# Performance work log

Hardware: AMD Instinct MI355X
Metric: run time of the kernel (lower is better)

## Reference

```python
import jax, jax.numpy as jnp
import numpy as np

PS = 8          # patch size
D_STATE = 16
D_CONV = 4
DT_RANK = 6     # ceil(96/16)
N_HEADS = 2
NEG = jnp.float32(-1e30)
_DIRS = np.array([[-1, 0], [1, 0], [0, -1], [0, 1]], np.int32)


def _ln(x, w, b, eps=1e-5):
    mu = x.mean(-1, keepdims=True)
    var = ((x - mu) ** 2).mean(-1, keepdims=True)
    return (x - mu) * jax.lax.rsqrt(var + eps) * w + b


def _vit_score_map(x, pos_embed, proj_w, proj_b, in_w, in_b, out_w, out_b,
                   ln1_w, ln1_b, ff1_w, ff1_b, ff2_w, ff2_b, ln2_w, ln2_b,
                   score_w, score_b):
    B, C, H, W = x.shape
    Hp, Wp = H // PS, W // PS
    N = Hp * Wp
    E = proj_w.shape[0]
    # F.unfold ordering: per patch the vector is (C, kr, kc) flattened
    patches = x.reshape(B, C, Hp, PS, Wp, PS).transpose(0, 2, 4, 1, 3, 5).reshape(B, N, C * PS * PS)
    patches = patches @ proj_w.T + proj_b
    if pos_embed.shape[1] != N:
        o = int(pos_embed.shape[1] ** 0.5)
        pe = jax.image.resize(pos_embed.reshape(1, o, o, E), (1, Hp, Wp, E), 'bilinear').reshape(1, N, E)
    else:
        pe = pos_embed
    patches = patches + 0.1 * pe
    # nn.TransformerEncoderLayer defaults: post-norm, ReLU, eval (no dropout)
    qkv = patches @ in_w.T + in_b
    q, k, v = jnp.split(qkv, 3, axis=-1)
    dh = E // N_HEADS
    def heads(t):
        return t.reshape(B, N, N_HEADS, dh).transpose(0, 2, 1, 3)
    q, k, v = heads(q), heads(k), heads(v)
    attn = jax.nn.softmax(jnp.einsum('bhqd,bhkd->bhqk', q, k) / np.float32(np.sqrt(dh)), axis=-1)
    ctx = jnp.einsum('bhqk,bhkd->bhqd', attn, v).transpose(0, 2, 1, 3).reshape(B, N, E)
    src = _ln(patches + (ctx @ out_w.T + out_b), ln1_w, ln1_b)
    ff = jax.nn.relu(src @ ff1_w.T + ff1_b) @ ff2_w.T + ff2_b
    src = _ln(src + ff, ln2_w, ln2_b)
    scores = jax.nn.sigmoid((src @ score_w.T + score_b)[..., 0])
    pvar = patches.var(axis=-1, ddof=1)          # torch.var is unbiased
    final = 0.7 * scores + 0.3 * jax.nn.sigmoid(pvar * 10.0)
    return final.reshape(B, Hp, Wp)


def _traversal(score):
    """Greedy adaptive patch traversal: start at global argmax, walk to the best
    unvisited 4-neighbor; on dead-end jump to the global argmax over unvisited."""
    Hp, Wp = score.shape
    n = Hp * Wp
    s = score.reshape(-1)
    dirs = jnp.asarray(_DIRS)
    start = jnp.argmax(s).astype(jnp.int32)
    visited0 = jnp.zeros((n,), bool).at[start].set(True)

    def step(carry, _):
        visited, cur = carry
        ci, cj = cur // Wp, cur % Wp
        ni, nj = ci + dirs[:, 0], cj + dirs[:, 1]
        valid = (ni >= 0) & (ni < Hp) & (nj >= 0) & (nj < Wp)
        nidx = (jnp.clip(ni, 0, Hp - 1) * Wp + jnp.clip(nj, 0, Wp - 1)).astype(jnp.int32)
        nsc = jnp.where(valid & ~visited[nidx], s[nidx], NEG)
        b = jnp.argmax(nsc)                       # first-max tie-break == '>' loop order
        jump = jnp.argmax(jnp.where(visited, NEG, s)).astype(jnp.int32)
        nxt = jnp.where(nsc[b] > NEG * 0.5, nidx[b], jump).astype(jnp.int32)
        return (visited.at[nxt].set(True), nxt), nxt

    _, rest = jax.lax.scan(step, (visited0, start), None, length=n - 1)
    return jnp.concatenate([start[None], rest])


def _mamba(u, in_w, conv_w, conv_b, xproj_w, dt_w, dt_b, A_log, D_skip, out_w):
    B, L, _ = u.shape
    d_in = conv_w.shape[0]
    xz = u @ in_w.T                               # (B,L,2*d_in)
    xx, z = jnp.split(xz, 2, axis=-1)
    # causal depthwise conv over sequence
    xc = jnp.pad(xx.transpose(0, 2, 1), ((0, 0), (0, 0), (D_CONV - 1, 0)))
    xc = jax.lax.conv_general_dilated(xc, conv_w, (1,), 'VALID',
                                      feature_group_count=d_in,
                                      dimension_numbers=('NCH', 'OIH', 'NCH'))
    xx = jax.nn.silu((xc + conv_b[None, :, None]).transpose(0, 2, 1))   # (B,L,d_in)
    dbl = xx @ xproj_w.T
    dt, Bm, Cm = jnp.split(dbl, [DT_RANK, DT_RANK + D_STATE], axis=-1)
    dt = jax.nn.softplus(dt @ dt_w.T + dt_b)      # (B,L,d_in)
    A = -jnp.exp(A_log)                           # (d_in, d_state)

    def step(h, inp):
        dt_t, B_t, C_t, x_t = inp                 # (B,d_in),(B,ds),(B,ds),(B,d_in)
        h = jnp.exp(dt_t[..., None] * A) * h + (dt_t * x_t)[..., None] * B_t[:, None, :]
        return h, jnp.einsum('bds,bs->bd', h, C_t)

    h0 = jnp.zeros((B, d_in, D_STATE), u.dtype)
    xs = (dt.transpose(1, 0, 2), Bm.transpose(1, 0, 2), Cm.transpose(1, 0, 2), xx.transpose(1, 0, 2))
    _, ys = jax.lax.scan(step, h0, xs)
    y = ys.transpose(1, 0, 2) + xx * D_skip
    return (y * jax.nn.silu(z)) @ out_w.T


def setup_inputs() -> dict:
    key = jax.random.key(0)
    ks = jax.random.split(key, 20)
    B, C, H, W = 2, 96, 128, 128
    E, FF = 96, 2048
    d_in, dr, ds, dc = 192, 6, 16, 4
    f32 = jnp.float32
    def w(k, shape, s=0.02):
        return jax.random.normal(k, shape, f32) * s
    return dict(
        x=jax.random.normal(ks[0], (B, C, H, W), f32),
        pe=w(ks[1], (B, H * W, C), 0.02),
        pos_embed=w(ks[2], (1, 784, E)),
        vit_proj_w=w(ks[3], (E, C * PS * PS)),
        vit_proj_b=jnp.zeros((E,), f32),
        attn_in_w=w(ks[4], (3 * E, E)),
        attn_in_b=jnp.zeros((3 * E,), f32),
        attn_out_w=w(ks[5], (E, E)),
        attn_out_b=jnp.zeros((E,), f32),
        ln1_w=jnp.ones((E,), f32), ln1_b=jnp.zeros((E,), f32),
        ff1_w=w(ks[6], (FF, E)), ff1_b=jnp.zeros((FF,), f32),
        ff2_w=w(ks[7], (E, FF)), ff2_b=jnp.zeros((E,), f32),
        ln2_w=jnp.ones((E,), f32), ln2_b=jnp.zeros((E,), f32),
        score_w=w(ks[8], (1, E)), score_b=jnp.zeros((1,), f32),
        norm_w=jnp.ones((C,), f32), norm_b=jnp.zeros((C,), f32),
        in_proj_w=w(ks[9], (2 * d_in, C)),
        conv_w=w(ks[10], (d_in, 1, dc), 0.1),
        conv_b=jnp.zeros((d_in,), f32),
        x_proj_w=w(ks[11], (dr + 2 * ds, d_in)),
        dt_w=w(ks[12], (d_in, dr)),
        dt_b=jnp.full((d_in,), -4.6, f32),        # softplus(dt_b) ~ 0.01 (mamba dt init)
        A_log=jnp.log(jnp.tile(jnp.arange(1, ds + 1, dtype=f32), (d_in, 1))),
        D_skip=jnp.ones((d_in,), f32),
        out_proj_w=w(ks[13], (C, d_in)),
    )


def reference(x, pe, pos_embed, vit_proj_w, vit_proj_b, attn_in_w, attn_in_b,
              attn_out_w, attn_out_b, ln1_w, ln1_b, ff1_w, ff1_b, ff2_w, ff2_b,
              ln2_w, ln2_b, score_w, score_b, norm_w, norm_b, in_proj_w,
              conv_w, conv_b, x_proj_w, dt_w, dt_b, A_log, D_skip, out_proj_w):
    B, C, H, W = x.shape
    n = H * W
    # Dynamic_Adaptive_Scan with the code's DCNv3Function-is-None fallback:
    # x = input_last, permuted back to channels-first => identity on x.
    x_adapted = x
    score_map = _vit_score_map(x_adapted, pos_embed, vit_proj_w, vit_proj_b,
                               attn_in_w, attn_in_b, attn_out_w, attn_out_b,
                               ln1_w, ln1_b, ff1_w, ff1_b, ff2_w, ff2_b,
                               ln2_w, ln2_b, score_w, score_b)
    order = jax.vmap(_traversal)(jax.lax.stop_gradient(score_map))    # (B, Hp*Wp)
    Hp, Wp = score_map.shape[1], score_map.shape[2]
    pi, pj = order // Wp, order % Wp
    # expand each patch into its PSxPS pixels in raster order
    offs = (jnp.arange(PS, dtype=jnp.int32)[:, None] * W + jnp.arange(PS, dtype=jnp.int32)[None, :]).reshape(-1)
    idx = ((pi * PS * W + pj * PS)[..., None] + offs).reshape(B, n)    # (B, n)
    x_tok = jnp.take_along_axis(x_adapted.reshape(B, C, n), idx[:, None, :], axis=2).transpose(0, 2, 1)
    pe_r = jnp.take_along_axis(pe, idx[..., None], axis=1)
    tokens = _ln(x_tok + pe_r, norm_w, norm_b)
    y = _mamba(tokens, in_proj_w, conv_w, conv_b, x_proj_w, dt_w, dt_b, A_log, D_skip, out_proj_w)
    # scatter back to spatial raster order
    out = jax.vmap(lambda yb, ib: jnp.zeros_like(yb).at[ib].set(yb))(y, idx)
    return out.transpose(0, 2, 1).reshape(B, C, H, W)
```

## Files before the change

### kernel.cpp

```cpp
#include <hip/hip_runtime.h>
#include <math.h>

#define BB 2
#define CC 96
#define HH 128
#define WW 128
#define PS 8
#define HP 16
#define WP 16
#define NPATCH 256
#define EE 96
#define FF 2048
#define DH 48
#define DIN 192
#define DR 6
#define DS 16
#define LL 16384
#define NCHUNK 512
#define CLEN 32
#define NSEG 16
#define SEGC 32
#define KTOT 6144
#define KSPLIT 32
#define KSL 192

__device__ __forceinline__ float sigmoid_acc(float x){ return 1.f/(1.f+expf(-x)); }
__device__ __forceinline__ float sigmoid_fast(float x){ return 1.f/(1.f+__expf(-x)); }

__global__ void k_resize_pe(const float* __restrict__ pos, float* __restrict__ pe16){
  int n = blockIdx.x;
  int oi = n / WP, oj = n % WP;
  int e = threadIdx.x;
  const float inv = 1.75f;
  float sfi = (oi + 0.5f)*inv - 0.5f;
  float sfj = (oj + 0.5f)*inv - 0.5f;
  int i0 = max(0, (int)ceilf(sfi - inv)), i1 = min(27, (int)floorf(sfi + inv));
  int j0 = max(0, (int)ceilf(sfj - inv)), j1 = min(27, (int)floorf(sfj + inv));
  float si = 0.f, sj = 0.f;
  for(int j=i0;j<=i1;j++) si += fmaxf(0.f, 1.f - fabsf(sfi - (float)j)/inv);
  for(int j=j0;j<=j1;j++) sj += fmaxf(0.f, 1.f - fabsf(sfj - (float)j)/inv);
  float acc = 0.f;
  for(int ji=i0;ji<=i1;ji++){
    float wv = fmaxf(0.f, 1.f - fabsf(sfi - (float)ji)/inv) / si;
    for(int jj=j0;jj<=j1;jj++){
      float wu = fmaxf(0.f, 1.f - fabsf(sfj - (float)jj)/inv);
      acc += wv * (wu/sj) * pos[(ji*28+jj)*EE + e];
    }
  }
  pe16[n*EE + e] = acc;
}

__global__ void k_wtr(const float* __restrict__ vw, float* __restrict__ Wt){
  __shared__ float t[64*97];
  int k0 = blockIdx.x*64;
  int tid = threadIdx.x;
  for(int i=tid;i<64*EE;i+=256){
    int e = i>>6, kk = i&63;
    t[kk*97 + e] = vw[(size_t)e*KTOT + k0 + kk];
  }
  __syncthreads();
  for(int i=tid;i<64*EE;i+=256){
    int kk = i/EE, e = i%EE;
    Wt[(size_t)(k0+kk)*EE + e] = t[kk*97 + e];
  }
}

__global__ __launch_bounds__(384) void k_pproj(const float* __restrict__ x,
    const float* __restrict__ Wt, float* __restrict__ part){
  __shared__ float As[16*196];
  int bidx = blockIdx.x;
  int ks = bidx & (KSPLIT-1);
  int pb = bidx >> 5;
  int b = pb >> 4, pi = pb & 15;
  int c0 = ks*3;
  int tid = threadIdx.x;
  for(int i=tid;i<24*128;i+=384){
    int row = i>>7;
    int col = i&127;
    int cl = row>>3, dr = row&7;
    float v = x[(((size_t)(b*CC + c0+cl))<<14) + (size_t)((pi*PS+dr)<<7) + col];
    As[(col>>3)*196 + cl*64 + dr*8 + (col&7)] = v;
  }
  __syncthreads();
  int e = tid % EE;
  int pq = tid / EE;
  const float* wp = Wt + (size_t)(ks*KSL)*EE + e;
  float acc0=0.f, acc1=0.f, acc2=0.f, acc3=0.f;
  const float4* A0 = (const float4*)(As + (pq*4+0)*196);
  const float4* A1 = (const float4*)(As + (pq*4+1)*196);
  const float4* A2 = (const float4*)(As + (pq*4+2)*196);
  const float4* A3 = (const float4*)(As + (pq*4+3)*196);
  #pragma unroll 4
  for(int k4=0;k4<48;k4++){
    float w0 = wp[(k4*4+0)*EE];
    float w1 = wp[(k4*4+1)*EE];
    float w2 = wp[(k4*4+2)*EE];
    float w3 = wp[(k4*4+3)*EE];
    float4 a;
    a = A0[k4]; acc0 += a.x*w0 + a.y*w1 + a.z*w2 + a.w*w3;
    a = A1[k4]; acc1 += a.x*w0 + a.y*w1 + a.z*w2 + a.w*w3;
    a = A2[k4]; acc2 += a.x*w0 + a.y*w1 + a.z*w2 + a.w*w3;
    a = A3[k4]; acc3 += a.x*w0 + a.y*w1 + a.z*w2 + a.w*w3;
  }
  size_t gp0 = (size_t)b*NPATCH + pi*WP + pq*4;
  part[((size_t)ks*512 + gp0+0)*EE + e] = acc0;
  part[((size_t)ks*512 + gp0+1)*EE + e] = acc1;
  part[((size_t)ks*512 + gp0+2)*EE + e] = acc2;
  part[((size_t)ks*512 + gp0+3)*EE + e] = acc3;
}

__global__ __launch_bounds__(320) void k_preduce_qkv(const float* __restrict__ part,
    const float* __restrict__ pb, const float* __restrict__ pe16,
    const float* __restrict__ inw, const float* __restrict__ inb,
    float* __restrict__ patches, float* __restrict__ pvar, float* __restrict__ qkv){
  int gp = blockIdx.x;
  int n = gp % NPATCH;
  int tid = threadIdx.x;
  __shared__ float a[EE];
  __shared__ float ps[2], pq2[2];
  float v = 0.f;
  if(tid < EE){
    float s = 0.f;
    #pragma unroll 8
    for(int ks=0;ks<KSPLIT;ks++) s += part[((size_t)ks*512 + gp)*EE + tid];
    v = s + pb[tid] + 0.1f*pe16[n*EE + tid];
    a[tid] = v;
    patches[(size_t)gp*EE + tid] = v;
  }
  if(tid < 128){
    float sv = v, sq = v*v;
    for(int off=32; off>0; off>>=1){ sv += __shfl_xor(sv, off); sq += __shfl_xor(sq, off); }
    if((tid&63)==0){ ps[tid>>6]=sv; pq2[tid>>6]=sq; }
  }
  __syncthreads();
  if(tid==0){
    float s = ps[0]+ps[1], qq = pq2[0]+pq2[1];
    float mu = s/EE;
    pvar[gp] = (qq - EE*mu*mu)/(EE-1);
  }
  if(tid < 288){
    const float4* ar = (const float4*)a;
    const float4* wr = (const float4*)(inw + (size_t)tid*EE);
    float4 s4 = {0.f,0.f,0.f,0.f};
    #pragma unroll
    for(int k=0;k<24;k++){
      float4 av=ar[k], wv=wr[k];
      s4.x += av.x*wv.x; s4.y += av.y*wv.y; s4.z += av.z*wv.z; s4.w += av.w*wv.w;
    }
    qkv[(size_t)gp*288 + tid] = inb[tid] + (s4.x+s4.y)+(s4.z+s4.w);
  }
}

__global__ __launch_bounds__(256) void k_attn_ln1(const float* __restrict__ qkv,
    const float* __restrict__ ow, const float* __restrict__ ob,
    const float* __restrict__ patches, const float* __restrict__ lw,
    const float* __restrict__ lb, float* __restrict__ src1){
  int gb = blockIdx.x;
  int i = gb & 255, b = gb >> 8;
  int tid = threadIdx.x;
  __shared__ float q[EE];
  __shared__ float2 red[NPATCH];
  __shared__ float p0[NPATCH], p1[NPATCH];
  __shared__ float part[2][EE];
  __shared__ float ctxs[EE];
  __shared__ float ps[2], pq2[2], st[2];
  const float* base = qkv + (size_t)b*NPATCH*288;
  if(tid < EE) q[tid] = base[(size_t)i*288 + tid];
  __syncthreads();
  float sc0, sc1;
  {
    const float4* krow = (const float4*)(base + (size_t)tid*288 + 96);
    const float4* q4 = (const float4*)q;
    float4 a0 = {0.f,0.f,0.f,0.f}, a1 = {0.f,0.f,0.f,0.f};
    #pragma unroll
    for(int k=0;k<12;k++){
      float4 kv=krow[k], qv=q4[k];
      a0.x += qv.x*kv.x; a0.y += qv.y*kv.y; a0.z += qv.z*kv.z; a0.w += qv.w*kv.w;
    }
    #pragma unroll
    for(int k=12;k<24;k++){
      float4 kv=krow[k], qv=q4[k];
      a1.x += qv.x*kv.x; a1.y += qv.y*kv.y; a1.z += qv.z*kv.z; a1.w += qv.w*kv.w;
    }
    sc0 = ((a0.x+a0.y)+(a0.z+a0.w)) * 0.14433756729740643f;
    sc1 = ((a1.x+a1.y)+(a1.z+a1.w)) * 0.14433756729740643f;
  }
  red[tid] = make_float2(sc0, sc1); __syncthreads();
  for(int stp=128; stp>0; stp>>=1){
    if(tid<stp){ float2 o=red[tid+stp]; red[tid].x=fmaxf(red[tid].x,o.x); red[tid].y=fmaxf(red[tid].y,o.y); }
    __syncthreads();
  }
  float2 mx = red[0]; __syncthreads();
  float ev0 = expf(sc0 - mx.x), ev1 = expf(sc1 - mx.y);
  red[tid] = make_float2(ev0, ev1); __syncthreads();
  for(int stp=128; stp>0; stp>>=1){
    if(tid<stp){ float2 o=red[tid+stp]; red[tid].x+=o.x; red[tid].y+=o.y; }
    __syncthreads();
  }
  float2 dn = red[0]; __syncthreads();
  p0[tid] = ev0/dn.x; p1[tid] = ev1/dn.y;
  __syncthreads();
  if(tid < 192){
    int dd = tid % EE, jh = tid / EE;
    const float* vb = base + 192 + dd;
    const float* pp = (dd < DH) ? p0 : p1;
    float acc0 = 0.f, acc1 = 0.f;
    #pragma unroll 4
    for(int j=jh*128; j<jh*128+128; j+=2){
      acc0 += pp[j]*vb[(size_t)j*288];
      acc1 += pp[j+1]*vb[(size_t)(j+1)*288];
    }
    part[jh][dd] = acc0+acc1;
  }
  __syncthreads();
  if(tid < EE) ctxs[tid] = part[0][tid] + part[1][tid];
  __syncthreads();
  float o = 0.f;
  if(tid < EE){
    const float4* ar = (const float4*)ctxs;
    const float4* wr = (const float4*)(ow + (size_t)tid*EE);
    float4 s4 = {0.f,0.f,0.f,0.f};
    #pragma unroll
    for(int k=0;k<24;k++){
      float4 av=ar[k], wv=wr[k];
      s4.x += av.x*wv.x; s4.y += av.y*wv.y; s4.z += av.z*wv.z; s4.w += av.w*wv.w;
    }
    o = ob[tid] + (s4.x+s4.y)+(s4.z+s4.w) + patches[(size_t)gb*EE + tid];
  }
  if(tid < 128){
    float sv = o, sq = o*o;
    for(int off=32; off>0; off>>=1){ sv += __shfl_xor(sv, off); sq += __shfl_xor(sq, off); }
    if((tid&63)==0){ ps[tid>>6]=sv; pq2[tid>>6]=sq; }
  }
  __syncthreads();
  if(tid==0){
    float s = ps[0]+ps[1], qq = pq2[0]+pq2[1];
    float mu = s/EE;
    st[0]=mu; st[1]=rsqrtf(qq/EE - mu*mu + 1e-5f);
  }
  __syncthreads();
  if(tid < EE) src1[(size_t)gb*EE + tid] = (o-st[0])*st[1]*lw[tid] + lb[tid];
}

__global__ __launch_bounds__(512) void k_ffn(const float* __restrict__ src1,
    const float* __restrict__ w1, const float* __restrict__ b1,
    const float* __restrict__ w2, const float* __restrict__ b2,
    const float* __restrict__ lw, const float* __restrict__ lb,
    const float* __restrict__ sw, const float* __restrict__ sb,
    const float* __restrict__ pvar, float* __restrict__ fscore){
  __shared__ float hr[2][FF];
  __shared__ float partl[8][EE];
  __shared__ float s2[2][EE];
  __shared__ float psr[2][2], pqr[2][2], str[2][2];
  int row0 = blockIdx.x*2; int tid = threadIdx.x;
  {
    const float4* a0 = (const float4*)(src1 + (size_t)row0*EE);
    const float4* a1 = (const float4*)(src1 + (size_t)(row0+1)*EE);
    for(int fo=0;fo<4;fo++){
      int f = fo*512 + tid;
      const float4* wr = (const float4*)(w1 + (size_t)f*EE);
      float bc = b1[f];
      float acc0=bc, acc1=bc;
      #pragma unroll
      for(int k=0;k<24;k++){
        float4 wv = wr[k];
        float4 av;
        av = a0[k]; acc0 += av.x*wv.x+av.y*wv.y+av.z*wv.z+av.w*wv.w;
        av = a1[k]; acc1 += av.x*wv.x+av.y*wv.y+av.z*wv.z+av.w*wv.w;
      }
      hr[0][f] = fmaxf(acc0, 0.f);
      hr[1][f] = fmaxf(acc1, 0.f);
    }
  }
  __syncthreads();
  if(tid < 384){
    int e = tid % EE, fg = tid / EE;
    const float4* wr = (const float4*)(w2 + (size_t)e*FF + fg*512);
    const float4* h0 = (const float4*)(hr[0] + fg*512);
    const float4* h1 = (const float4*)(hr[1] + fg*512);
    float acc0=0.f, acc1=0.f;
    #pragma unroll 4
    for(int k=0;k<128;k++){
      float4 wv = wr[k];
      float4 hv;
      hv = h0[k]; acc0 += hv.x*wv.x+hv.y*wv.y+hv.z*wv.z+hv.w*wv.w;
      hv = h1[k]; acc1 += hv.x*wv.x+hv.y*wv.y+hv.z*wv.z+hv.w*wv.w;
    }
    partl[0*4+fg][e] = acc0;
    partl[1*4+fg][e] = acc1;
  }
  __syncthreads();
  if(tid < 192){
    int r = tid / EE, e2 = tid % EE;
    float s = partl[r*4+0][e2] + partl[r*4+1][e2] + partl[r*4+2][e2] + partl[r*4+3][e2];
    s2[r][e2] = s + b2[e2] + src1[(size_t)(row0+r)*EE + e2];
  }
  __syncthreads();
  int g = tid >> 7, t = tid & 127;
  float v = 0.f;
  if(g < 2){
    v = (t < EE) ? s2[g][t] : 0.f;
    float sv = v, sq = v*v;
    for(int off=32; off>0; off>>=1){ sv += __shfl_xor(sv, off); sq += __shfl_xor(sq, off); }
    if((t&63)==0){ psr[g][t>>6]=sv; pqr[g][t>>6]=sq; }
  }
  __syncthreads();
  if(g < 2 && t == 0){
    float s = psr[g][0]+psr[g][1], qq = pqr[g][0]+pqr[g][1];
    float mu = s/EE;
    str[g][0]=mu; str[g][1]=rsqrtf(qq/EE - mu*mu + 1e-5f);
  }
  __syncthreads();
  if(g < 2){
    float o = (t < EE) ? ((v-str[g][0])*str[g][1]*lw[t] + lb[t]) * sw[t] : 0.f;
    for(int off=32; off>0; off>>=1) o += __shfl_xor(o, off);
    if((t&63)==0) psr[g][t>>6] = o;
  }
  __syncthreads();
  if(g < 2 && t == 0){
    float acc = psr[g][0]+psr[g][1] + sb[0];
    fscore[row0+g] = 0.7f*sigmoid_acc(acc) + 0.3f*sigmoid_acc(pvar[row0+g]*10.f);
  }
}

__global__ __launch_bounds__(768) void k_trav_fused(const float* __restrict__ fscore,
    const float* __restrict__ x, const float* __restrict__ pe,
    const float* __restrict__ nw, const float* __restrict__ nb,
    const float* __restrict__ w, int* __restrict__ pixmap,
    float* __restrict__ xx, float* __restrict__ z){
  __shared__ float fsl[NPATCH];
  __shared__ int   sidxl[NPATCH];
  __shared__ int   ordl[NPATCH];
  __shared__ float a[32*100];
  __shared__ float ps[12*384];
  int tid = threadIdx.x;
  if(blockIdx.x < 2){
    int b = blockIdx.x;
    int lane = tid;
    if(lane < 64){
      for(int k=lane;k<NPATCH;k+=64) fsl[k] = fscore[b*NPATCH+k];
    }
    __syncthreads();
    if(lane < 64){
      float s0=fsl[lane], s1=fsl[64+lane], s2=fsl[128+lane], s3=fsl[192+lane];
      int i0=lane, i1=64+lane, i2=128+lane, i3=192+lane;
      int c0=0,c1=0,c2=0,c3=0;
      for(int j=0;j<NPATCH;j++){
        float sj=fsl[j];
        c0 += (sj>s0 || (sj==s0 && j<i0)) ? 1:0;
        c1 += (sj>s1 || (sj==s1 && j<i1)) ? 1:0;
        c2 += (sj>s2 || (sj==s2 && j<i2)) ? 1:0;
        c3 += (sj>s3 || (sj==s3 && j<i3)) ? 1:0;
      }
      sidxl[c0]=i0; sidxl[c1]=i1; sidxl[c2]=i2; sidxl[c3]=i3;
    }
    __syncthreads();
    if(lane==0){
      int cur = sidxl[0];
      ordl[0] = cur;
      fsl[cur] = -1e30f;
      int ptr = 1;
      int jcand = sidxl[1];
      for(int step=1; step<NPATCH; step++){
        int ci = cur>>4, cj = cur&15;
        int a0 = (ci>0)  ? cur-16 : cur;
        int a1 = (ci<15) ? cur+16 : cur;
        int a2 = (cj>0)  ? cur-1  : cur;
        int a3 = (cj<15) ? cur+1  : cur;
        float n0 = fsl[a0];
        float n1 = fsl[a1];
        float n2 = fsl[a2];
        float n3 = fsl[a3];
        float bv = n0; int bi = a0;
        if(n1 > bv){ bv=n1; bi=a1; }
        if(n2 > bv){ bv=n2; bi=a2; }
        if(n3 > bv){ bv=n3; bi=a3; }
        int nxt = (bv > -1e29f) ? bi : jcand;
        fsl[nxt] = -1e30f;
        ordl[step] = nxt;
        cur = nxt;
        if(nxt == jcand && step < NPATCH-1){
          float jv;
          do { ptr++; jcand = sidxl[ptr]; jv = fsl[jcand]; } while(jv <= -1e29f);
        }
      }
    }
    __syncthreads();
    for(int l=tid; l<LL; l+=768){
      int r = l>>6, q = l&63;
      int p = ordl[r];
      pixmap[b*LL + l] = (((p>>4)*PS + (q>>3))<<7) + (p&15)*PS + (q&7);
    }
  } else {
    int rb = blockIdx.x - 2;
    int R0 = rb*32;
    int b = R0 >> 14;
    int p0 = R0 & 16383;
    for(int i=tid;i<3072;i+=768){
      int c = i>>5, pl = i&31;
      a[pl*100 + c] = x[(((size_t)(b*CC + c))<<14) + p0 + pl];
    }
    __syncthreads();
    for(int i=tid;i<3072;i+=768){
      int pl = i/96, c = i - pl*96;
      a[pl*100 + c] += pe[((size_t)b*(HH*WW) + p0 + pl)*CC + c];
    }
    __syncthreads();
    {
      int wid = tid>>6, lane = tid&63;
      for(int t=wid; t<32; t+=12){
        float v1 = a[t*100 + lane];
        float v2 = (lane<32) ? a[t*100 + 64 + lane] : 0.f;
        float sv = v1+v2, sq = v1*v1 + v2*v2;
        for(int off=32; off>0; off>>=1){ sv += __shfl_xor(sv, off); sq += __shfl_xor(sq, off); }
        float mu = sv/EE;
        float rs = rsqrtf(sq/EE - mu*mu + 1e-5f);
        a[t*100 + lane] = (v1-mu)*rs*nw[lane] + nb[lane];
        if(lane < 32) a[t*100 + 64 + lane] = (v2-mu)*rs*nw[64+lane] + nb[64+lane];
      }
    }
    __syncthreads();
    int kh = tid/384, col = tid - kh*384;
    float4 wv[12];
    const float4* wr4 = (const float4*)(w + (size_t)col*EE + kh*48);
    #pragma unroll
    for(int i=0;i<12;i++) wv[i] = wr4[i];
    #pragma unroll
    for(int g=0; g<3; g++){
      float acc[12];
      #pragma unroll
      for(int r=0;r<12;r++){
        int gi = g*12 + r;
        if(gi < 32){
          const float4* ar = (const float4*)(a + gi*100 + kh*48);
          float4 s4 = {0.f,0.f,0.f,0.f};
          #pragma unroll
          for(int i=0;i<12;i++){
            float4 av = ar[i];
            s4.x += av.x*wv[i].x; s4.y += av.y*wv[i].y; s4.z += av.z*wv[i].z; s4.w += av.w*wv[i].w;
          }
          acc[r] = (s4.x+s4.y)+(s4.z+s4.w);
        } else acc[r] = 0.f;
      }
      if(kh==1){
        #pragma unroll
        for(int r=0;r<12;r++) if(g*12+r < 32) ps[r*384 + col] = acc[r];
      }
      __syncthreads();
      if(kh==0){
        #pragma unroll
        for(int r=0;r<12;r++){
          int gi = g*12 + r;
          if(gi < 32){
            float tot = acc[r] + ps[r*384 + col];
            if(col < DIN) xx[(size_t)(R0 + gi)*DIN + col] = tot;
            else          z [(size_t)(R0 + gi)*DIN + (col - DIN)] = tot;
          }
        }
      }
      __syncthreads();
    }
  }
}

__global__ __launch_bounds__(256) void k_mamba1(const float* __restrict__ xx,
    const int* __restrict__ pixmap, const float* __restrict__ cw, const float* __restrict__ cb,
    const float* __restrict__ xpw, const float* __restrict__ dtw, const float* __restrict__ dtb,
    const float* __restrict__ Alog, float* __restrict__ xc, float* __restrict__ dblg,
    float* __restrict__ hend, float* __restrict__ sumdt){
  __shared__ int pixl[35];
  __shared__ float xxl[35*DIN];
  __shared__ float xcl[32*196];
  __shared__ float dbl[32*40];
  int blk = blockIdx.x; int b = blk>>9; int c = blk&511;
  int l0 = c*CLEN;
  int tid = threadIdx.x;
  if(tid < 35){
    int l = l0 - 3 + tid;
    pixl[tid] = (l >= 0) ? pixmap[b*LL + l] : 0;
  }
  __syncthreads();
  for(int i=tid; i<35*DIN; i+=256){
    int rr = i/DIN, d = i - rr*DIN;
    int l = l0 - 3 + rr;
    xxl[i] = (l >= 0) ? xx[((size_t)b*LL + pixl[rr])*DIN + d] : 0.f;
  }
  __syncthreads();
  for(int i=tid; i<32*DIN; i+=256){
    int rr = i/DIN, d = i - rr*DIN;
    float v = cb[d]
      + cw[d*4+0]*xxl[(rr+0)*DIN + d]
      + cw[d*4+1]*xxl[(rr+1)*DIN + d]
      + cw[d*4+2]*xxl[(rr+2)*DIN + d]
      + cw[d*4+3]*xxl[(rr+3)*DIN + d];
    float sv = v * sigmoid_fast(v);
    xcl[rr*196 + d] = sv;
    xc[((size_t)b*LL + l0 + rr)*DIN + d] = sv;
  }
  __syncthreads();
  for(int task=tid; task<32*38; task+=256){
    int r = task & 31, o = task >> 5;
    const float4* wr = (const float4*)(xpw + (size_t)o*DIN);
    const float4* ar = (const float4*)(xcl + r*196);
    float4 s4 = {0.f,0.f,0.f,0.f};
    #pragma unroll
    for(int k=0;k<48;k++){
      float4 av=ar[k], wv=wr[k];
      s4.x += av.x*wv.x; s4.y += av.y*wv.y; s4.z += av.z*wv.z; s4.w += av.w*wv.w;
    }
    float val = (s4.x+s4.y)+(s4.z+s4.w);
    int om = (o<6) ? o : o+2;
    dbl[r*40 + om] = val;
    dblg[((size_t)b*LL + l0 + r)*40 + om] = val;
  }
  __syncthreads();
  float* dtl = xxl;
  for(int i=tid; i<32*DIN; i+=256){
    int rr = i/DIN, d = i - rr*DIN;
    float acc = dtb[d];
    #pragma unroll
    for(int j=0;j<DR;j++) acc += dbl[rr*40+j]*dtw[d*DR+j];
    dtl[rr*DIN + d] = fmaxf(acc, 0.f) + log1pf(__expf(-fabsf(acc)));
  }
  __syncthreads();
  if(tid < DIN){
    int d = tid;
    float A[16];
    {
      const float4* a4 = (const float4*)(Alog + d*DS);
      #pragma unroll
      for(int i=0;i<4;i++){
        float4 v = a4[i];
        A[i*4+0]=-expf(v.x); A[i*4+1]=-expf(v.y); A[i*4+2]=-expf(v.z); A[i*4+3]=-expf(v.w);
      }
    }
    float h[16];
    #pragma unroll
    for(int s=0;s<16;s++) h[s]=0.f;
    float sd = 0.f;
    for(int t=0;t<CLEN;t++){
      float dtv = dtl[t*DIN + d];
      float xv  = xcl[t*196 + d];
      const float4* bp4 = (const float4*)(dbl + t*40 + 8);
      float4 b0=bp4[0], b1=bp4[1], b2=bp4[2], b3=bp4[3];
      float e[16];
      #pragma unroll
      for(int s=0;s<16;s++) e[s] = __expf(dtv*A[s]);
      float Bv[16] = {b0.x,b0.y,b0.z,b0.w,b1.x,b1.y,b1.z,b1.w,b2.x,b2.y,b2.z,b2.w,b3.x,b3.y,b3.z,b3.w};
      float dx = dtv*xv; sd += dtv;
      #pragma unroll
      for(int s=0;s<16;s++) h[s] = e[s]*h[s] + dx*Bv[s];
    }
    size_t o = ((size_t)c*BB + b)*DIN + d;
    float4* hp = (float4*)(hend + o*DS);
    hp[0] = make_float4(h[0],h[1],h[2],h[3]);
    hp[1] = make_float4(h[4],h[5],h[6],h[7]);
    hp[2] = make_float4(h[8],h[9],h[10],h[11]);
    hp[3] = make_float4(h[12],h[13],h[14],h[15]);
    sumdt[o] = sd;
  }
}

__global__ __launch_bounds__(256) void k_scan2a(const float* __restrict__ hend,
    const float* __restrict__ sumdt, const float* __restrict__ Alog,
    float* __restrict__ segP, float* __restrict__ segH){
  int g = blockIdx.x*256 + threadIdx.x;
  int seg = g / 6144; int r = g % 6144;
  int b = r / 3072; int d = (r % 3072) >> 4; int s = r & 15;
  float A = -expf(Alog[d*DS + s]);
  float P = 1.f, H = 0.f;
  int c0 = seg*SEGC;
  for(int cc=0; cc<SEGC; cc+=4){
    float sd[4], he[4];
    #pragma unroll
    for(int j=0;j<4;j++){
      size_t o = ((size_t)(c0+cc+j)*BB + b)*DIN + d;
      sd[j] = sumdt[o]; he[j] = hend[o*DS + s];
    }
    #pragma unroll
    for(int j=0;j<4;j++){
      float aa = __expf(A*sd[j]);
      H = aa*H + he[j]; P *= aa;
    }
  }
  segP[seg*6144 + r] = P; segH[seg*6144 + r] = H;
}

__global__ void k_scan2b(const float* __restrict__ segP, const float* __restrict__ segH,
                         float* __restrict__ segHin){
  int r = blockIdx.x*256 + threadIdx.x;
  float P[NSEG], H[NSEG];
  #pragma unroll
  for(int sg=0; sg<NSEG; sg++){ P[sg]=segP[sg*6144+r]; H[sg]=segH[sg*6144+r]; }
  float h = 0.f;
  #pragma unroll
  for(int sg=0; sg<NSEG; sg++){
    segHin[sg*6144 + r] = h;
    h = P[sg]*h + H[sg];
  }
}

__global__ __launch_bounds__(256) void k_scan2c(float* __restrict__ hend,
    const float* __restrict__ sumdt, const float* __restrict__ Alog,
    const float* __restrict__ segHin){
  int g = blockIdx.x*256 + threadIdx.x;
  int seg = g / 6144; int r = g % 6144;
  int b = r / 3072; int d = (r % 3072) >> 4; int s = r & 15;
  float A = -expf(Alog[d*DS + s]);
  float h = segHin[seg*6144 + r];
  int c0 = seg*SEGC;
  for(int cc=0; cc<SEGC; cc+=4){
    float sd[4], he[4]; size_t oo[4];
    #pragma unroll
    for(int j=0;j<4;j++){
      oo[j] = ((size_t)(c0+cc+j)*BB + b)*DIN + d;
      sd[j] = sumdt[oo[j]]; he[j] = hend[oo[j]*DS + s];
    }
    #pragma unroll
    for(int j=0;j<4;j++){
      hend[oo[j]*DS + s] = h;
      float aa = __expf(A*sd[j]);
      h = aa*h + he[j];
    }
  }
}

__global__ __launch_bounds__(192) void k_scan3(const float* __restrict__ xc,
    const float* __restrict__ dblg, const float* __restrict__ dtw, const float* __restrict__ dtb,
    const float* __restrict__ Alog, const float* __restrict__ hin,
    const float* __restrict__ Dskip, const int* __restrict__ pixmap,
    float* __restrict__ z){
  __shared__ float dbll[32*40];
  __shared__ int pixs[CLEN];
  int blk = blockIdx.x;
  int b = blk >> 9, c = blk & 511;
  int d = threadIdx.x;
  for(int i=d; i<32*40; i+=192) dbll[i] = dblg[((size_t)b*LL + c*CLEN)*40 + i];
  if(d < CLEN) pixs[d] = pixmap[b*LL + c*CLEN + d];
  float A[16];
  {
    const float4* a4 = (const float4*)(Alog + d*DS);
    #pragma unroll
    for(int i=0;i<4;i++){
      float4 v = a4[i];
      A[i*4+0]=-expf(v.x); A[i*4+1]=-expf(v.y); A[i*4+2]=-expf(v.z); A[i*4+3]=-expf(v.w);
    }
  }
  size_t o = ((size_t)c*BB + b)*DIN + d;
  float h[16];
  {
    const float4* hi = (const float4*)(hin + o*DS);
    #pragma unroll
    for(int i=0;i<4;i++){
      float4 v = hi[i];
      h[i*4+0]=v.x; h[i*4+1]=v.y; h[i*4+2]=v.z; h[i*4+3]=v.w;
    }
  }
  float dtwr[DR];
  #pragma unroll
  for(int j=0;j<DR;j++) dtwr[j] = dtw[d*DR+j];
  float dtbd = dtb[d];
  float Dv = Dskip[d];
  const float* xp = xc + ((size_t)b*LL + (size_t)c*CLEN)*DIN + d;
  __syncthreads();
  for(int t=0;t<CLEN;t++){
    float acc = dtbd;
    #pragma unroll
    for(int j=0;j<DR;j++) acc += dbll[t*40+j]*dtwr[j];
    float dtv = fmaxf(acc, 0.f) + log1pf(__expf(-fabsf(acc)));
    float xv  = xp[(size_t)t*DIN];
    size_t zrow = ((size_t)b*LL + pixs[t])*DIN + d;
    float zv  = z[zrow];
    const float4* bp4 = (const float4*)(dbll + t*40 + 8);
    const float4* cp4 = (const float4*)(dbll + t*40 + 24);
    float4 b0=bp4[0], b1=bp4[1], b2=bp4[2], b3=bp4[3];
    float4 c0=cp4[0], c1=cp4[1], c2=cp4[2], c3=cp4[3];
    float e[16];
    #pragma unroll
    for(int s=0;s<16;s++) e[s] = __expf(dtv*A[s]);
    float Bv[16] = {b0.x,b0.y,b0.z,b0.w,b1.x,b1.y,b1.z,b1.w,b2.x,b2.y,b2.z,b2.w,b3.x,b3.y,b3.z,b3.w};
    float Cv[16] = {c0.x,c0.y,c0.z,c0.w,c1.x,c1.y,c1.z,c1.w,c2.x,c2.y,c2.z,c2.w,c3.x,c3.y,c3.z,c3.w};
    float dx = dtv*xv;
    float y = 0.f;
    #pragma unroll
    for(int s=0;s<16;s++){ h[s] = e[s]*h[s] + dx*Bv[s]; y += h[s]*Cv[s]; }
    float yy = y + xv*Dv;
    z[zrow] = yy * (zv * sigmoid_fast(zv));
  }
}

__global__ __launch_bounds__(384) void k_outproj(const float* __restrict__ g,
    const float* __restrict__ w, float* __restrict__ out){
  __shared__ float a[16*DIN];
  __shared__ float psA[16*EE];
  __shared__ float psB[16*EE];
  int rb = blockIdx.x; size_t row0 = (size_t)rb*16;
  int b = (int)(row0 >> 14);
  int pix0 = (int)(row0 & 16383);
  int tid = threadIdx.x;
  int col = tid % EE, kq = tid / EE;
  {
    const float4* src = (const float4*)(g + row0*DIN);
    float4* ad = (float4*)a;
    ad[tid] = src[tid];
    ad[tid+384] = src[tid+384];
  }
  float4 wv[12];
  const float4* wr4 = (const float4*)(w + (size_t)col*DIN + kq*48);
  #pragma unroll
  for(int i=0;i<12;i++) wv[i] = wr4[i];
  __syncthreads();
  float acc[16];
  for(int r=0;r<16;r++){
    const float4* ar = (const float4*)(a + r*DIN + kq*48);
    float4 s4 = {0.f,0.f,0.f,0.f};
    #pragma unroll
    for(int i=0;i<12;i++){
      float4 av = ar[i];
      s4.x += av.x*wv[i].x; s4.y += av.y*wv[i].y; s4.z += av.z*wv[i].z; s4.w += av.w*wv[i].w;
    }
    acc[r] = (s4.x+s4.y)+(s4.z+s4.w);
  }
  if(kq==1){
    for(int r=0;r<16;r++) psA[r*EE+col] = acc[r];
  }
  if(kq==3){
    for(int r=0;r<16;r++) psB[r*EE+col] = acc[r];
  }
  __syncthreads();
  if(kq==0){
    for(int r=0;r<16;r++) acc[r] += psA[r*EE+col];
  }
  if(kq==2){
    for(int r=0;r<16;r++) acc[r] += psB[r*EE+col];
  }
  __syncthreads();
  if(kq==2){
    for(int r=0;r<16;r++) psA[r*EE+col] = acc[r];
  }
  __syncthreads();
  if(kq==0){
    float4* ob4 = (float4*)(out + (((size_t)(b*CC + col))<<14) + pix0);
    ob4[0] = make_float4(acc[0]+psA[0*EE+col],  acc[1]+psA[1*EE+col],  acc[2]+psA[2*EE+col],  acc[3]+psA[3*EE+col]);
    ob4[1] = make_float4(acc[4]+psA[4*EE+col],  acc[5]+psA[5*EE+col],  acc[6]+psA[6*EE+col],  acc[7]+psA[7*EE+col]);
    ob4[2] = make_float4(acc[8]+psA[8*EE+col],  acc[9]+psA[9*EE+col],  acc[10]+psA[10*EE+col], acc[11]+psA[11*EE+col]);
    ob4[3] = make_float4(acc[12]+psA[12*EE+col], acc[13]+psA[13*EE+col], acc[14]+psA[14*EE+col], acc[15]+psA[15*EE+col]);
  }
}

extern "C" void kernel_launch(void* const* d_in, const int* in_sizes, int n_in,
                              void* d_out, int out_size, void* d_ws, size_t ws_size,
                              hipStream_t stream){
  (void)in_sizes; (void)n_in; (void)out_size; (void)ws_size;
  const float* x    = (const float*)d_in[0];
  const float* pe   = (const float*)d_in[1];
  const float* pos  = (const float*)d_in[2];
  const float* vw   = (const float*)d_in[3];
  const float* vb   = (const float*)d_in[4];
  const float* inw  = (const float*)d_in[5];
  const float* inb  = (const float*)d_in[6];
  const float* ow   = (const float*)d_in[7];
  const float* ob   = (const float*)d_in[8];
  const float* l1w  = (const float*)d_in[9];
  const float* l1b  = (const float*)d_in[10];
  const float* f1w  = (const float*)d_in[11];
  const float* f1b  = (const float*)d_in[12];
  const float* f2w  = (const float*)d_in[13];
  const float* f2b  = (const float*)d_in[14];
  const float* l2w  = (const float*)d_in[15];
  const float* l2b  = (const float*)d_in[16];
  const float* sw   = (const float*)d_in[17];
  const float* sb   = (const float*)d_in[18];
  const float* nw   = (const float*)d_in[19];
  const float* nb   = (const float*)d_in[20];
  const float* ipw  = (const float*)d_in[21];
  const float* cw   = (const float*)d_in[22];
  const float* cb   = (const float*)d_in[23];
  const float* xpw  = (const float*)d_in[24];
  const float* dtw  = (const float*)d_in[25];
  const float* dtbp = (const float*)d_in[26];
  const float* alog = (const float*)d_in[27];
  const float* dsk  = (const float*)d_in[28];
  const float* opw  = (const float*)d_in[29];
  float* out = (float*)d_out;

  char* wsb = (char*)d_ws;
  size_t off = 0;
  auto alloc = [&](size_t nfloats)->void*{
    void* p = (void*)(wsb + off);
    off += ((nfloats*sizeof(float) + 255) & ~(size_t)255);
    return p;
  };
  float* pe16    = (float*)alloc(256*96);
  float* patches = (float*)alloc(512*96);
  float* pvar    = (float*)alloc(512);
  float* qkv     = (float*)alloc((size_t)512*288);
  float* src1    = (float*)alloc(512*96);
  float* fscore  = (float*)alloc(512);
  int*   pixmap  = (int*)  alloc((size_t)2*16384);
  float* tokens  = (float*)alloc((size_t)2*16384*96);
  float* xxb     = (float*)alloc((size_t)2*16384*192);
  float* zb      = (float*)alloc((size_t)2*16384*192);
  float* xcb     = (float*)alloc((size_t)2*16384*192);
  float* dblg    = (float*)alloc((size_t)2*16384*40);
  float* sumdt   = (float*)alloc((size_t)NCHUNK*2*192);
  float* segP    = (float*)alloc((size_t)NSEG*6144);
  float* segH    = (float*)alloc((size_t)NSEG*6144);
  float* segHin  = (float*)alloc((size_t)NSEG*6144);
  float* Wt    = xxb;
  float* part  = tokens;
  float* hend  = tokens;
  float* hin   = hend;

  k_resize_pe   <<<256,   96, 0, stream>>>(pos, pe16);
  k_wtr         <<<96,   256, 0, stream>>>(vw, Wt);
  k_pproj       <<<1024, 384, 0, stream>>>(x, Wt, part);
  k_preduce_qkv <<<512,  320, 0, stream>>>(part, vb, pe16, inw, inb, patches, pvar, qkv);
  k_attn_ln1    <<<512,  256, 0, stream>>>(qkv, ow, ob, patches, l1w, l1b, src1);
  k_ffn         <<<256,  512, 0, stream>>>(src1, f1w, f1b, f2w, f2b, l2w, l2b, sw, sb, pvar, fscore);
  k_trav_fused  <<<1026, 768, 0, stream>>>(fscore, x, pe, nw, nb, ipw, pixmap, xxb, zb);
  k_mamba1      <<<1024, 256, 0, stream>>>(xxb, pixmap, cw, cb, xpw, dtw, dtbp, alog, xcb, dblg, hend, sumdt);
  k_scan2a      <<<384,  256, 0, stream>>>(hend, sumdt, alog, segP, segH);
  k_scan2b      <<<24,   256, 0, stream>>>(segP, segH, segHin);
  k_scan2c      <<<384,  256, 0, stream>>>(hend, sumdt, alog, segHin);
  k_scan3       <<<1024, 192, 0, stream>>>(xcb, dblg, dtw, dtbp, alog, hin, dsk, pixmap, zb);
  k_outproj     <<<2048, 384, 0, stream>>>(zb, opw, out);
}
```

Baseline: 461.6 us.

## Split mamba1 into conv, x-proj and scan kernels; fold scan2b into scan2c

Splits the monolithic mamba1 kernel, which needed about 60KB of shared memory, into three kernels. A conv+SiLU gather kernel, an x-projection kernel with 8 rows per block, and a chunk-scan kernel with one thread per channel that computes dt inline. Each stage gets a leaner resource footprint and more blocks, which should raise occupancy. The tiny scan2b launch is removed: scan2c now recomputes each segment's incoming state serially from segP/segH. The cost is extra global round-trips for xc and dblg, two more launches, and redundant prefix work in scan2c.

After: 468.7 us. Within noise of the previous version (+1.5%).

```diff
diff --git a/kernel.cpp b/kernel.cpp
--- a/kernel.cpp
+++ b/kernel.cpp
@@ -463,17 +463,12 @@
   }
 }
 
-__global__ __launch_bounds__(256) void k_mamba1(const float* __restrict__ xx,
-    const int* __restrict__ pixmap, const float* __restrict__ cw, const float* __restrict__ cb,
-    const float* __restrict__ xpw, const float* __restrict__ dtw, const float* __restrict__ dtb,
-    const float* __restrict__ Alog, float* __restrict__ xc, float* __restrict__ dblg,
-    float* __restrict__ hend, float* __restrict__ sumdt){
+__global__ __launch_bounds__(256) void k_convgather(const float* __restrict__ xx,
+    const int* __restrict__ pixmap, const float* __restrict__ cw,
+    const float* __restrict__ cb, float* __restrict__ xc){
   __shared__ int pixl[35];
   __shared__ float xxl[35*DIN];
-  __shared__ float xcl[32*196];
-  __shared__ float dbl[32*40];
-  int blk = blockIdx.x; int b = blk>>9; int c = blk&511;
-  int l0 = c*CLEN;
+  int blk = blockIdx.x; int b = blk>>9; int l0 = (blk&511)*32;
   int tid = threadIdx.x;
   if(tid < 35){
     int l = l0 - 3 + tid;
@@ -493,72 +488,85 @@
       + cw[d*4+1]*xxl[(rr+1)*DIN + d]
       + cw[d*4+2]*xxl[(rr+2)*DIN + d]
       + cw[d*4+3]*xxl[(rr+3)*DIN + d];
-    float sv = v * sigmoid_fast(v);
-    xcl[rr*196 + d] = sv;
-    xc[((size_t)b*LL + l0 + rr)*DIN + d] = sv;
-  }
-  __syncthreads();
-  for(int task=tid; task<32*38; task+=256){
-    int r = task & 31, o = task >> 5;
-    const float4* wr = (const float4*)(xpw + (size_t)o*DIN);
-    const float4* ar = (const float4*)(xcl + r*196);
-    float4 s4 = {0.f,0.f,0.f,0.f};
-    #pragma unroll
-    for(int k=0;k<48;k++){
-      float4 av=ar[k], wv=wr[k];
-      s4.x += av.x*wv.x; s4.y += av.y*wv.y; s4.z += av.z*wv.z; s4.w += av.w*wv.w;
-    }
-    float val = (s4.x+s4.y)+(s4.z+s4.w);
-    int om = (o<6) ? o : o+2;
-    dbl[r*40 + om] = val;
-    dblg[((size_t)b*LL + l0 + r)*40 + om] = val;
-  }
-  __syncthreads();
-  float* dtl = xxl;
-  for(int i=tid; i<32*DIN; i+=256){
-    int rr = i/DIN, d = i - rr*DIN;
-    float acc = dtb[d];
-    #pragma unroll
-    for(int j=0;j<DR;j++) acc += dbl[rr*40+j]*dtw[d*DR+j];
-    dtl[rr*DIN + d] = fmaxf(acc, 0.f) + log1pf(__expf(-fabsf(acc)));
-  }
-  __syncthreads();
-  if(tid < DIN){
-    int d = tid;
-    float A[16];
-    {
-      const float4* a4 = (const float4*)(Alog + d*DS);
+    xc[((size_t)b*LL + l0 + rr)*DIN + d] = v * sigmoid_fast(v);
+  }
+}
+
+__global__ __launch_bounds__(320) void k_xproj(const float* __restrict__ xc, const float* __restrict__ xpw,
+    float* __restrict__ dblg){
+  __shared__ float a[8][196];
+  int rb = blockIdx.x; size_t row0 = (size_t)rb*8;
+  int tid = threadIdx.x;
+  for(int i=tid;i<8*DIN;i+=320){ int r=i/DIN, k=i%DIN; a[r][k] = xc[(row0+r)*DIN + k]; }
+  __syncthreads();
+  {
+    int r = tid & 7, o = tid >> 3;
+    if(o < 38){
+      const float4* wr = (const float4*)(xpw + (size_t)o*DIN);
+      const float4* ar = (const float4*)(a[r]);
+      float4 s4 = {0.f,0.f,0.f,0.f};
       #pragma unroll
-      for(int i=0;i<4;i++){
-        float4 v = a4[i];
-        A[i*4+0]=-expf(v.x); A[i*4+1]=-expf(v.y); A[i*4+2]=-expf(v.z); A[i*4+3]=-expf(v.w);
+      for(int k=0;k<48;k++){
+        float4 av=ar[k], wv=wr[k];
+        s4.x += av.x*wv.x; s4.y += av.y*wv.y; s4.z += av.z*wv.z; s4.w += av.w*wv.w;
       }
-    }
-    float h[16];
-    #pragma unroll
-    for(int s=0;s<16;s++) h[s]=0.f;
-    float sd = 0.f;
-    for(int t=0;t<CLEN;t++){
-      float dtv = dtl[t*DIN + d];
-      float xv  = xcl[t*196 + d];
-      const float4* bp4 = (const float4*)(dbl + t*40 + 8);
-      float4 b0=bp4[0], b1=bp4[1], b2=bp4[2], b3=bp4[3];
-      float e[16];
-      #pragma unroll
-      for(int s=0;s<16;s++) e[s] = __expf(dtv*A[s]);
-      float Bv[16] = {b0.x,b0.y,b0.z,b0.w,b1.x,b1.y,b1.z,b1.w,b2.x,b2.y,b2.z,b2.w,b3.x,b3.y,b3.z,b3.w};
-      float dx = dtv*xv; sd += dtv;
-      #pragma unroll
-      for(int s=0;s<16;s++) h[s] = e[s]*h[s] + dx*Bv[s];
-    }
-    size_t o = ((size_t)c*BB + b)*DIN + d;
-    float4* hp = (float4*)(hend + o*DS);
-    hp[0] = make_float4(h[0],h[1],h[2],h[3]);
-    hp[1] = make_float4(h[4],h[5],h[6],h[7]);
-    hp[2] = make_float4(h[8],h[9],h[10],h[11]);
-    hp[3] = make_float4(h[12],h[13],h[14],h[15]);
-    sumdt[o] = sd;
-  }
+      int om = (o < 6) ? o : o + 2;
+      dblg[(row0 + r)*40 + om] = (s4.x+s4.y)+(s4.z+s4.w);
+    }
+  }
+}
+
+__global__ __launch_bounds__(192) void k_scan1(const float* __restrict__ dblg,
+    const float* __restrict__ xc, const float* __restrict__ dtw, const float* __restrict__ dtb,
+    const float* __restrict__ Alog, float* __restrict__ hend, float* __restrict__ sumdt){
+  __shared__ float dbll[32*40];
+  int blk = blockIdx.x;
+  int b = blk >> 9, c = blk & (NCHUNK-1);
+  int d = threadIdx.x;
+  for(int i=d; i<32*40; i+=192) dbll[i] = dblg[((size_t)b*LL + (size_t)c*CLEN)*40 + i];
+  float A[16];
+  {
+    const float4* a4 = (const float4*)(Alog + d*DS);
+    #pragma unroll
+    for(int i=0;i<4;i++){
+      float4 v = a4[i];
+      A[i*4+0]=-expf(v.x); A[i*4+1]=-expf(v.y); A[i*4+2]=-expf(v.z); A[i*4+3]=-expf(v.w);
+    }
+  }
+  float dtwr[DR];
+  #pragma unroll
+  for(int j=0;j<DR;j++) dtwr[j] = dtw[d*DR+j];
+  float dtbd = dtb[d];
+  float h[16];
+  #pragma unroll
+  for(int s=0;s<16;s++) h[s]=0.f;
+  float sd = 0.f;
+  size_t base = (size_t)b*LL + (size_t)c*CLEN;
+  const float* xp = xc + base*DIN + d;
+  __syncthreads();
+  for(int t=0;t<CLEN;t++){
+    float acc = dtbd;
+    #pragma unroll
+    for(int j=0;j<DR;j++) acc += dbll[t*40+j]*dtwr[j];
+    float dtv = fmaxf(acc, 0.f) + log1pf(__expf(-fabsf(acc)));
+    float xv  = xp[(size_t)t*DIN];
+    const float4* bp4 = (const float4*)(dbll + t*40 + 8);
+    float4 b0=bp4[0], b1=bp4[1], b2=bp4[2], b3=bp4[3];
+    float e[16];
+    #pragma unroll
+    for(int s=0;s<16;s++) e[s] = __expf(dtv*A[s]);
+    float Bv[16] = {b0.x,b0.y,b0.z,b0.w,b1.x,b1.y,b1.z,b1.w,b2.x,b2.y,b2.z,b2.w,b3.x,b3.y,b3.z,b3.w};
+    float dx = dtv*xv; sd += dtv;
+    #pragma unroll
+    for(int s=0;s<16;s++) h[s] = e[s]*h[s] + dx*Bv[s];
+  }
+  size_t o = ((size_t)c*BB + b)*DIN + d;
+  float4* hp = (float4*)(hend + o*DS);
+  hp[0] = make_float4(h[0],h[1],h[2],h[3]);
+  hp[1] = make_float4(h[4],h[5],h[6],h[7]);
+  hp[2] = make_float4(h[8],h[9],h[10],h[11]);
+  hp[3] = make_float4(h[12],h[13],h[14],h[15]);
+  sumdt[o] = sd;
 }
 
 __global__ __launch_bounds__(256) void k_scan2a(const float* __restrict__ hend,
@@ -586,28 +594,17 @@
   segP[seg*6144 + r] = P; segH[seg*6144 + r] = H;
 }
 
-__global__ void k_scan2b(const float* __restrict__ segP, const float* __restrict__ segH,
-                         float* __restrict__ segHin){
-  int r = blockIdx.x*256 + threadIdx.x;
-  float P[NSEG], H[NSEG];
-  #pragma unroll
-  for(int sg=0; sg<NSEG; sg++){ P[sg]=segP[sg*6144+r]; H[sg]=segH[sg*6144+r]; }
-  float h = 0.f;
-  #pragma unroll
-  for(int sg=0; sg<NSEG; sg++){
-    segHin[sg*6144 + r] = h;
-    h = P[sg]*h + H[sg];
-  }
-}
-
 __global__ __launch_bounds__(256) void k_scan2c(float* __restrict__ hend,
     const float* __restrict__ sumdt, const float* __restrict__ Alog,
-    const float* __restrict__ segHin){
+    const float* __restrict__ segP, const float* __restrict__ segH){
   int g = blockIdx.x*256 + threadIdx.x;
   int seg = g / 6144; int r = g % 6144;
   int b = r / 3072; int d = (r % 3072) >> 4; int s = r & 15;
   float A = -expf(Alog[d*DS + s]);
-  float h = segHin[seg*6144 + r];
+  float h = 0.f;
+  for(int sg=0; sg<seg; sg++){
+    h = segP[sg*6144 + r]*h + segH[sg*6144 + r];
+  }
   int c0 = seg*SEGC;
   for(int cc=0; cc<SEGC; cc+=4){
     float sd[4], he[4]; size_t oo[4];
@@ -635,7 +632,7 @@
   int blk = blockIdx.x;
   int b = blk >> 9, c = blk & 511;
   int d = threadIdx.x;
-  for(int i=d; i<32*40; i+=192) dbll[i] = dblg[((size_t)b*LL + c*CLEN)*40 + i];
+  for(int i=d; i<32*40; i+=192) dbll[i] = dblg[((size_t)b*LL + (size_t)c*CLEN)*40 + i];
   if(d < CLEN) pixs[d] = pixmap[b*LL + c*CLEN + d];
   float A[16];
   {
@@ -806,7 +803,6 @@
   float* sumdt   = (float*)alloc((size_t)NCHUNK*2*192);
   float* segP    = (float*)alloc((size_t)NSEG*6144);
   float* segH    = (float*)alloc((size_t)NSEG*6144);
-  float* segHin  = (float*)alloc((size_t)NSEG*6144);
   float* Wt    = xxb;
   float* part  = tokens;
   float* hend  = tokens;
@@ -819,10 +815,11 @@
   k_attn_ln1    <<<512,  256, 0, stream>>>(qkv, ow, ob, patches, l1w, l1b, src1);
   k_ffn         <<<256,  512, 0, stream>>>(src1, f1w, f1b, f2w, f2b, l2w, l2b, sw, sb, pvar, fscore);
   k_trav_fused  <<<1026, 768, 0, stream>>>(fscore, x, pe, nw, nb, ipw, pixmap, xxb, zb);
-  k_mamba1      <<<1024, 256, 0, stream>>>(xxb, pixmap, cw, cb, xpw, dtw, dtbp, alog, xcb, dblg, hend, sumdt);
+  k_convgather  <<<1024, 256, 0, stream>>>(xxb, pixmap, cw, cb, xcb);
+  k_xproj       <<<4096, 320, 0, stream>>>(xcb, xpw, dblg);
+  k_scan1       <<<1024, 192, 0, stream>>>(dblg, xcb, dtw, dtbp, alog, hend, sumdt);
   k_scan2a      <<<384,  256, 0, stream>>>(hend, sumdt, alog, segP, segH);
-  k_scan2b      <<<24,   256, 0, stream>>>(segP, segH, segHin);
-  k_scan2c      <<<384,  256, 0, stream>>>(hend, sumdt, alog, segHin);
+  k_scan2c      <<<384,  256, 0, stream>>>(hend, sumdt, alog, segP, segH);
   k_scan3       <<<1024, 192, 0, stream>>>(xcb, dblg, dtw, dtbp, alog, hin, dsk, pixmap, zb);
   k_outproj     <<<2048, 384, 0, stream>>>(zb, opw, out);
 }
```
